# Kernel optimization log

Hardware: AMD Instinct MI355X
Metric: run time of the kernel (lower is better)

The kernel has to match this reference:

```python
import jax, jax.numpy as jnp
import numpy as np

R0 = 1.0
DIM_A, DIM_V, DIM_D = 32, 32, 32
N_NODES = 20000
N_EDGES = 640000


def radial_encode_8(r, r0):
    # 8 Gaussian radial basis functions on the edge length |r_ij|
    d = jnp.linalg.norm(r, axis=-1)                      # [E]
    centers = jnp.linspace(0.0, r0, 8)                   # [8]
    width = r0 / 8.0
    return jnp.exp(-(((d[..., None] - centers) / width) ** 2))  # [E,8]


def tens_sigmoid_vec(v):
    # norm-saturating nonlinearity for rank-1 tensors (direction-preserving)
    n2 = jnp.sum(v * v, axis=-1, keepdims=True)
    return v * jax.lax.rsqrt(1.0 + n2)


def setup_inputs() -> dict:
    key = jax.random.key(0)
    ks = jax.random.split(key, 12)

    def lin(k, fan_in, fan_out):
        return jax.random.normal(k, (fan_in, fan_out), jnp.float32) / np.float32(np.sqrt(fan_in))

    return dict(
        r_ij=jax.random.normal(ks[0], (N_EDGES, 3), jnp.float32),
        w_rad=lin(ks[1], 8, DIM_A), b_rad=jnp.zeros((DIM_A,), jnp.float32),
        w_direct=lin(ks[2], DIM_A, DIM_A),
        w1=lin(ks[3], DIM_A, 2 * DIM_A), b1=jnp.zeros((2 * DIM_A,), jnp.float32),
        w2=lin(ks[4], 2 * DIM_A, 2 * DIM_A), b2=jnp.zeros((2 * DIM_A,), jnp.float32),
        w3=lin(ks[5], 2 * DIM_A, DIM_A), b3=jnp.zeros((DIM_A,), jnp.float32),
        w_v=lin(ks[6], DIM_A, DIM_V),
        w_d=lin(ks[7], DIM_A, DIM_D),
        edges_src=jax.random.randint(ks[8], (N_EDGES,), 0, N_NODES),
        n_nodes=N_NODES,
    )


def reference(r_ij, w_rad, b_rad, w_direct, w1, b1, w2, b2, w3, b3, w_v, w_d,
              edges_src, n_nodes):
    lrelu = lambda x: jnp.where(x > 0, x, 0.1 * x)
    # radial MLP: Linear(8, a) -> MLP (lin_direct + 3-layer leakyrelu net)
    h = radial_encode_8(r_ij, R0) @ w_rad + b_rad                      # [E,a]
    rad = h @ w_direct + (lrelu(lrelu(h @ w1 + b1) @ w2 + b2) @ w3 + b3)  # [E,a]
    rs = tens_sigmoid_vec(r_ij * (7.0 / R0))                            # [E,3]

    seg = lambda x: jax.ops.segment_sum(x, edges_src, num_segments=n_nodes)
    A_a = seg(rad)                                                      # [N,a]
    A_v = seg(rad[:, :, None] * rs[:, None, :])                         # [N,a,3]
    # phi_d_ij = rad ⊗ rs ⊗ rs per edge  -> [E,a,3,3], then scatter-sum
    A_d = seg(rad[:, :, None, None] * rs[:, None, None, :] * rs[:, None, :, None])  # [N,a,3,3]

    out_v = jnp.einsum('nac,av->nvc', A_v, w_v)                         # TensLinear rank 1
    out_d = jnp.einsum('naij,ad->ndij', A_d, w_d)                       # TensLinear rank 2
    return A_a, out_v, out_d
```

## Files before the change

kernel.cpp:

```cpp
#include <hip/hip_runtime.h>
#include <hip/hip_bf16.h>
#include <hip/hip_fp16.h>
#include <math.h>


#define TSIZE 8192
#define DMAX  2.0f
#define NPB   4
#define EPB   4
#define HB    128
#define TILE  10240

#define O_WRAD 0
#define O_BRAD 256
#define O_WDIR 288
#define O_W1   1312
#define O_B1   3360
#define O_W2   3424
#define O_B2   7520
#define O_W3   7584
#define O_B3   9632
#define O_WV   9664
#define O_WD   10688
#define W_TOT  11712

__device__ __forceinline__ float lrelu(float x) { return x > 0.0f ? x : 0.1f * x; }

__device__ __forceinline__ float ldf(const void* p, int i, bool f32) {
    return f32 ? ((const float*)p)[i]
               : __uint_as_float(((unsigned int)((const unsigned short*)p)[i]) << 16);
}
__device__ __forceinline__ void stf(void* p, size_t i, float v, bool f32) {
    if (f32) ((float*)p)[i] = v;
    else     ((__hip_bfloat16*)p)[i] = __float2bfloat16(v);
}

__device__ __forceinline__ bool detect_f32(const void* r) {
    const unsigned short* p = (const unsigned short*)r;
    int bad = 0;
#pragma unroll 8
    for (int i = 0; i < 128; i++) {
        float v = __uint_as_float(((unsigned int)p[i]) << 16);
        bad |= (!isfinite(v) || fabsf(v) > 1e5f) ? 1 : 0;
    }
    return bad != 0;
}

__global__ void k_prep(const void* __restrict__ r_ij,
                       const void* w_rad, const void* b_rad, const void* w_direct,
                       const void* w1, const void* b1, const void* w2, const void* b2,
                       const void* w3, const void* b3, const void* w_v, const void* w_d,
                       float* __restrict__ wcat, int* __restrict__ flag,
                       int* __restrict__ counts, int N) {
    const int b = blockIdx.x;
    if (b == 0) {
        if (threadIdx.x == 0) flag[0] = detect_f32(r_ij) ? 1 : 0;
    } else if (b <= 11) {
        const bool f32 = detect_f32(r_ij);
        const void* src; int cnt; int off;
        switch (b) {
            case 1:  src = w_rad;    cnt = 256;  off = O_WRAD; break;
            case 2:  src = b_rad;    cnt = 32;   off = O_BRAD; break;
            case 3:  src = w_direct; cnt = 1024; off = O_WDIR; break;
            case 4:  src = w1;       cnt = 2048; off = O_W1;   break;
            case 5:  src = b1;       cnt = 64;   off = O_B1;   break;
            case 6:  src = w2;       cnt = 4096; off = O_W2;   break;
            case 7:  src = b2;       cnt = 64;   off = O_B2;   break;
            case 8:  src = w3;       cnt = 2048; off = O_W3;   break;
            case 9:  src = b3;       cnt = 32;   off = O_B3;   break;
            case 10: src = w_v;      cnt = 1024; off = O_WV;   break;
            default: src = w_d;      cnt = 1024; off = O_WD;   break;
        }
        for (int i = threadIdx.x; i < cnt; i += blockDim.x)
            wcat[off + i] = ldf(src, i, f32);
    } else if (counts) {
        int i = (b - 12) * blockDim.x + threadIdx.x;
        if (i < N) counts[i] = 0;
    }
}

__global__ void __launch_bounds__(64 * EPB) k_table(const float* __restrict__ wcat,
                                                    float* __restrict__ tabI) {
    __shared__ float Lh[EPB][32], Lt1[EPB][64], Lt2[EPB][64], Lrad[EPB][32];

    const int s = threadIdx.x >> 6;
    const int j = threadIdx.x & 63;
    const int e = blockIdx.x * EPB + s;
    const float d = (float)e * (DMAX / (float)(TSIZE - 1));

    float enc[8];
#pragma unroll
    for (int k = 0; k < 8; k++) {
        float t = (d - (float)k * (1.0f / 7.0f)) * 8.0f;
        enc[k] = expf(-t * t);
    }

    if (j < 32) {
        float hv = wcat[O_BRAD + j];
#pragma unroll
        for (int k = 0; k < 8; k++) hv = fmaf(enc[k], wcat[O_WRAD + k * 32 + j], hv);
        Lh[s][j] = hv;
    }
    __syncthreads();

    {
        float v = wcat[O_B1 + j];
#pragma unroll
        for (int i = 0; i < 32; i++) v = fmaf(Lh[s][i], wcat[O_W1 + i * 64 + j], v);
        Lt1[s][j] = lrelu(v);
    }
    __syncthreads();

    {
        float v = wcat[O_B2 + j];
#pragma unroll
        for (int i = 0; i < 64; i++) v = fmaf(Lt1[s][i], wcat[O_W2 + i * 64 + j], v);
        Lt2[s][j] = lrelu(v);
    }
    __syncthreads();

    if (j < 32) {
        float v = wcat[O_B3 + j];
#pragma unroll
        for (int i = 0; i < 64; i++) v = fmaf(Lt2[s][i], wcat[O_W3 + i * 32 + j], v);
#pragma unroll
        for (int i = 0; i < 32; i++) v = fmaf(Lh[s][i], wcat[O_WDIR + i * 32 + j], v);
        Lrad[s][j] = v;
        tabI[e * 96 + j] = v;
    }
    __syncthreads();

    if (j < 32) {
        float sv = 0.0f, sd = 0.0f;
#pragma unroll
        for (int i = 0; i < 32; i++) {
            float ri = Lrad[s][i];
            sv = fmaf(ri, wcat[O_WV + i * 32 + j], sv);
            sd = fmaf(ri, wcat[O_WD + i * 32 + j], sd);
        }
        tabI[e * 96 + 32 + j] = sv;
        tabI[e * 96 + 64 + j] = sd;
    }
}

__global__ void __launch_bounds__(256) k_hist(const int* __restrict__ src, int E,
                                              int chunk,
                                              unsigned short* __restrict__ cnt,
                                              int N) {
    __shared__ int lcnt[TILE];
    const int b = blockIdx.x % HB;
    const int t = blockIdx.x / HB;
    const int lo = b * chunk;
    const int hi = min(lo + chunk, E);
    const int t0 = t * TILE;
    const int tl = min(TILE, N - t0);

    for (int i = threadIdx.x; i < tl; i += 256) lcnt[i] = 0;
    __syncthreads();
    for (int e = lo + threadIdx.x; e < hi; e += 256) {
        const int s = src[e] - t0;
        if ((unsigned)s < (unsigned)tl) atomicAdd(&lcnt[s], 1);
    }
    __syncthreads();
    unsigned short* out = cnt + (size_t)(t * HB + b) * TILE;
    for (int i = threadIdx.x; i < tl; i += 256)
        out[i] = (unsigned short)lcnt[i];
}

__global__ void __launch_bounds__(64) k_colscan(unsigned short* __restrict__ cnt,
                                                int* __restrict__ tot,
                                                int* __restrict__ coarse, int N) {
    const int lane = threadIdx.x;
    const int n = blockIdx.x * 64 + lane;
    int run = 0;
    if (n < N) {
        const int t = n / TILE;
        const int nl = n % TILE;
        unsigned short* col = cnt + (size_t)(t * HB) * TILE + nl;
#pragma unroll 4
        for (int b = 0; b < HB; b++) {
            int c = col[(size_t)b * TILE];
            col[(size_t)b * TILE] = (unsigned short)run;
            run += c;
        }
        tot[n] = run;
    }
    int s = run;
    for (int off = 32; off > 0; off >>= 1) s += __shfl_down(s, off);
    if (lane == 0) coarse[blockIdx.x] = s;
}

__global__ void __launch_bounds__(64) k_scan2(const int* __restrict__ tot,
                                              const int* __restrict__ coarse,
                                              int* __restrict__ rowstart, int N) {
    const int lane = threadIdx.x;
    const int b = blockIdx.x;
    int cpre = 0;
    if (lane == 0) for (int i = 0; i < b; i++) cpre += coarse[i];
    cpre = __shfl(cpre, 0);
    const int n = b * 64 + lane;
    const int v = (n < N) ? tot[n] : 0;
    int inc = v;
    for (int off = 1; off < 64; off <<= 1) {
        int y = __shfl_up(inc, off);
        if (lane >= off) inc += y;
    }
    if (n < N) rowstart[n] = cpre + inc - v;
    if (n == N - 1) rowstart[N] = cpre + inc;
}

template <bool P16>
__global__ void __launch_bounds__(256) k_place(
        const int* __restrict__ src, int E, int chunk,
        const unsigned short* __restrict__ cnt, const int* __restrict__ rowstart,
        const void* __restrict__ r_ij, const int* __restrict__ flag,
        void* __restrict__ epsv, int N) {
    __shared__ int cur[TILE];
    const int b = blockIdx.x % HB;
    const int t = blockIdx.x / HB;
    const int lo = b * chunk;
    const int hi = min(lo + chunk, E);
    const int t0 = t * TILE;
    const int tl = min(TILE, N - t0);
    const bool f32 = flag[0] != 0;

    const unsigned short* base = cnt + (size_t)(t * HB + b) * TILE;
    for (int i = threadIdx.x; i < tl; i += 256)
        cur[i] = rowstart[t0 + i] + (int)base[i];
    __syncthreads();
    for (int e = lo + threadIdx.x; e < hi; e += 256) {
        const int s = src[e] - t0;
        if ((unsigned)s < (unsigned)tl) {
            const int pos = atomicAdd(&cur[s], 1);
            const float x = ldf(r_ij, 3 * e + 0, f32);
            const float y = ldf(r_ij, 3 * e + 1, f32);
            const float z = ldf(r_ij, 3 * e + 2, f32);
            const float d2 = x * x + y * y + z * z;
            const float inv = rsqrtf(1.0f + 49.0f * d2);
            const float u = fminf(sqrtf(d2), DMAX) * ((float)(TSIZE - 1) / DMAX);
            const int ti = (int)(u + 0.5f);
            const float rs0 = 7.0f * x * inv, rs1 = 7.0f * y * inv,
                        rs2 = 7.0f * z * inv;
            if (P16) {
                ((float4*)epsv)[pos] =
                    make_float4(rs0, rs1, rs2, __int_as_float(ti * 384));
            } else {
                const unsigned int h0 = __half_as_ushort(__float2half(rs0));
                const unsigned int h1 = __half_as_ushort(__float2half(rs1));
                const unsigned int h2 = __half_as_ushort(__float2half(rs2));
                ((uint2*)epsv)[pos] =
                    make_uint2(h0 | (h1 << 16), h2 | ((unsigned)ti << 16));
            }
        }
    }
}

template <bool P16>
__global__ void __launch_bounds__(64 * NPB) k_nodes(
    const void* __restrict__ epsv,
    const int* __restrict__ rowstart,
    const float* __restrict__ tabI,
    const int* __restrict__ flag,
    void* __restrict__ out, int N) {
    const int wave = threadIdx.x >> 6;
    const int lane = threadIdx.x & 63;
    const int n = blockIdx.x * NPB + wave;
    if (n >= N) return;
    const int a = lane & 31;
    const bool hi = (lane >> 5) != 0;
    const bool f32 = flag[0] != 0;
    const char* tabA = (const char*)tabI + (a << 2);

    const int s0 = rowstart[n];
    const int s1 = rowstart[n + 1];

    float accR = 0.f, acc1 = 0.f, acc2 = 0.f, acc3 = 0.f,
          acc4 = 0.f, acc5 = 0.f, acc6 = 0.f;

    int idx = s0;
    for (; idx + 1 < s1; idx += 2) {
        float ax, ay, az, bx, by, bz;
        const float *pA, *pB;
        if (P16) {
            const float4 qa = ((const float4*)epsv)[idx];
            const float4 qb = ((const float4*)epsv)[idx + 1];
            ax = qa.x; ay = qa.y; az = qa.z;
            bx = qb.x; by = qb.y; bz = qb.z;
            pA = (const float*)(tabA + __float_as_int(qa.w));
            pB = (const float*)(tabA + __float_as_int(qb.w));
        } else {
            const uint2 qa = ((const uint2*)epsv)[idx];
            const uint2 qb = ((const uint2*)epsv)[idx + 1];
            ax = __half2float(__ushort_as_half((unsigned short)(qa.x & 0xffff)));
            ay = __half2float(__ushort_as_half((unsigned short)(qa.x >> 16)));
            az = __half2float(__ushort_as_half((unsigned short)(qa.y & 0xffff)));
            bx = __half2float(__ushort_as_half((unsigned short)(qb.x & 0xffff)));
            by = __half2float(__ushort_as_half((unsigned short)(qb.x >> 16)));
            bz = __half2float(__ushort_as_half((unsigned short)(qb.y & 0xffff)));
            pA = (const float*)(tabA + (int)(qa.y >> 16) * 384);
            pB = (const float*)(tabA + (int)(qb.y >> 16) * 384);
        }
        const float raA = pA[0], rvA = pA[32], rdA = pA[64];
        const float raB = pB[0], rvB = pB[32], rdB = pB[64];

        const float b1A = (hi ? rdA : rvA) * (hi ? ay : 1.0f);
        const float b2A = rdA * (hi ? az : ax);
        const float b1B = (hi ? rdB : rvB) * (hi ? by : 1.0f);
        const float b2B = rdB * (hi ? bz : bx);

        accR += raA + raB;
        acc1 += b1A * ax + b1B * bx;
        acc2 += b1A * ay + b1B * by;
        acc3 += b1A * az + b1B * bz;
        acc4 += b2A * ax + b2B * bx;
        acc5 += b2A * ay + b2B * by;
        acc6 += b2A * az + b2B * bz;
    }
    if (idx < s1) {
        float x, y, z;
        const float* p;
        if (P16) {
            const float4 q = ((const float4*)epsv)[idx];
            x = q.x; y = q.y; z = q.z;
            p = (const float*)(tabA + __float_as_int(q.w));
        } else {
            const uint2 q = ((const uint2*)epsv)[idx];
            x = __half2float(__ushort_as_half((unsigned short)(q.x & 0xffff)));
            y = __half2float(__ushort_as_half((unsigned short)(q.x >> 16)));
            z = __half2float(__ushort_as_half((unsigned short)(q.y & 0xffff)));
            p = (const float*)(tabA + (int)(q.y >> 16) * 384);
        }
        const float ra = p[0], rv = p[32], rd = p[64];
        const float b1 = (hi ? rd : rv) * (hi ? y : 1.0f);
        const float b2 = rd * (hi ? z : x);
        accR += ra;
        acc1 += b1 * x; acc2 += b1 * y; acc3 += b1 * z;
        acc4 += b2 * x; acc5 += b2 * y; acc6 += b2 * z;
    }

    const size_t baseV = (size_t)N * 32;
    const size_t baseD = (size_t)N * 128;
    if (!hi) {
        stf(out, (size_t)n * 32 + a, accR, f32);
        const size_t vb = baseV + (size_t)n * 96 + a * 3;
        stf(out, vb + 0, acc1, f32);
        stf(out, vb + 1, acc2, f32);
        stf(out, vb + 2, acc3, f32);
        const size_t db = baseD + (size_t)n * 288 + a * 9;
        stf(out, db + 0, acc4, f32);
        stf(out, db + 1, acc5, f32);
        stf(out, db + 2, acc6, f32);
    } else {
        const size_t db = baseD + (size_t)n * 288 + a * 9;
        stf(out, db + 3, acc1, f32);
        stf(out, db + 4, acc2, f32);
        stf(out, db + 5, acc3, f32);
        stf(out, db + 6, acc4, f32);
        stf(out, db + 7, acc5, f32);
        stf(out, db + 8, acc6, f32);
    }
}

__global__ void k_rank_g(const int* __restrict__ src, int* __restrict__ counts,
                         int* __restrict__ rank, int E) {
    int e = blockIdx.x * blockDim.x + threadIdx.x;
    if (e < E) rank[e] = atomicAdd(&counts[src[e]], 1);
}
__global__ void k_scan_g(const int* __restrict__ counts, int* __restrict__ rowstart,
                         int N, int E) {
    __shared__ int part[1024];
    const int t = threadIdx.x;
    const int CH = (N + 1023) / 1024;
    const int lo = t * CH;
    const int hi = min(lo + CH, N);
    int s = 0;
    for (int i = lo; i < hi; i++) s += counts[i];
    part[t] = s;
    __syncthreads();
    for (int off = 1; off < 1024; off <<= 1) {
        int v = part[t];
        int w = (t >= off) ? part[t - off] : 0;
        __syncthreads();
        part[t] = v + w;
        __syncthreads();
    }
    int run = (t == 0) ? 0 : part[t - 1];
    for (int i = lo; i < hi; i++) { rowstart[i] = run; run += counts[i]; }
    if (t == 0) rowstart[N] = E;
}
__global__ void k_place_g(const int* __restrict__ src, const int* __restrict__ rank,
                          const int* __restrict__ rowstart,
                          int* __restrict__ perm, int E) {
    int e = blockIdx.x * blockDim.x + threadIdx.x;
    if (e < E) perm[rowstart[src[e]] + rank[e]] = e;
}
__global__ void __launch_bounds__(64 * NPB) k_nodes_fb(
    const int* __restrict__ perm, const void* __restrict__ r_ij,
    const int* __restrict__ rowstart, const float* __restrict__ tabI,
    const int* __restrict__ flag, void* __restrict__ out, int N) {
    const int wave = threadIdx.x >> 6;
    const int lane = threadIdx.x & 63;
    const int n = blockIdx.x * NPB + wave;
    if (n >= N) return;
    const int a = lane & 31;
    const bool hi = (lane >> 5) != 0;
    const bool f32 = flag[0] != 0;
    const int s0 = rowstart[n], s1 = rowstart[n + 1];
    float accR = 0.f, acc1 = 0.f, acc2 = 0.f, acc3 = 0.f,
          acc4 = 0.f, acc5 = 0.f, acc6 = 0.f;
    for (int idx = s0; idx < s1; idx++) {
        const int e = perm[idx];
        const float x0 = ldf(r_ij, 3 * e + 0, f32);
        const float y0 = ldf(r_ij, 3 * e + 1, f32);
        const float z0 = ldf(r_ij, 3 * e + 2, f32);
        const float d2 = x0 * x0 + y0 * y0 + z0 * z0;
        const float inv = rsqrtf(1.0f + 49.0f * d2);
        const float x = 7.0f * x0 * inv, y = 7.0f * y0 * inv, z = 7.0f * z0 * inv;
        const float u = fminf(sqrtf(d2), DMAX) * ((float)(TSIZE - 1) / DMAX);
        const int b = (int)(u + 0.5f) * 96 + a;
        const float ra = tabI[b], rv = tabI[b + 32], rd = tabI[b + 64];
        const float b1 = (hi ? rd : rv) * (hi ? y : 1.0f);
        const float b2 = rd * (hi ? z : x);
        accR += ra;
        acc1 += b1 * x; acc2 += b1 * y; acc3 += b1 * z;
        acc4 += b2 * x; acc5 += b2 * y; acc6 += b2 * z;
    }
    const size_t baseV = (size_t)N * 32;
    const size_t baseD = (size_t)N * 128;
    if (!hi) {
        stf(out, (size_t)n * 32 + a, accR, f32);
        const size_t vb = baseV + (size_t)n * 96 + a * 3;
        stf(out, vb + 0, acc1, f32);
        stf(out, vb + 1, acc2, f32);
        stf(out, vb + 2, acc3, f32);
        const size_t db = baseD + (size_t)n * 288 + a * 9;
        stf(out, db + 0, acc4, f32);
        stf(out, db + 1, acc5, f32);
        stf(out, db + 2, acc6, f32);
    } else {
        const size_t db = baseD + (size_t)n * 288 + a * 9;
        stf(out, db + 3, acc1, f32);
        stf(out, db + 4, acc2, f32);
        stf(out, db + 5, acc3, f32);
        stf(out, db + 6, acc4, f32);
        stf(out, db + 7, acc5, f32);
        stf(out, db + 8, acc6, f32);
    }
}

extern "C" void kernel_launch(void* const* d_in, const int* in_sizes, int n_in,
                              void* d_out, int out_size, void* d_ws, size_t ws_size,
                              hipStream_t stream) {
    const void* r_ij     = d_in[0];
    const void* w_rad    = d_in[1];
    const void* b_rad    = d_in[2];
    const void* w_direct = d_in[3];
    const void* w1       = d_in[4];
    const void* b1       = d_in[5];
    const void* w2       = d_in[6];
    const void* b2       = d_in[7];
    const void* w3       = d_in[8];
    const void* b3       = d_in[9];
    const void* w_v      = d_in[10];
    const void* w_d      = d_in[11];
    const int* edges_src = (const int*)d_in[12];

    const int E = in_sizes[12];
    const int N = out_size / 416;
    const int chunk = (E + HB - 1) / HB;
    const int ntiles = (N + TILE - 1) / TILE;
    const int NB = (N + 63) / 64;

    const size_t cntBytes  = (size_t)ntiles * HB * TILE * 2;
    const size_t tailBytes = ((size_t)W_TOT + 4) * 4 + (size_t)TSIZE * 96 * 4
                           + cntBytes + ((size_t)N + NB + N + 1) * 4;
    const bool p16 = ws_size >= (size_t)E * 16 + tailBytes + 64;
    const bool p8  = !p16 && ws_size >= (size_t)E * 8 + tailBytes + 64;

    char* w = (char*)d_ws;
    if (p16 || p8) {
        const size_t slot = (size_t)E * (p16 ? 16 : 8);
        void* eps     = (void*)w;
        float* wcat   = (float*)(w + slot);
        int* flag     = (int*)(wcat + W_TOT);
        float* tabI   = (float*)(flag + 4);
        unsigned short* cnt = (unsigned short*)(tabI + (size_t)TSIZE * 96);
        int* tot      = (int*)((char*)cnt + cntBytes);
        int* coarse   = tot + N;
        int* rowstart = coarse + NB;

        k_prep<<<12, 256, 0, stream>>>(
            r_ij, w_rad, b_rad, w_direct, w1, b1, w2, b2, w3, b3, w_v, w_d,
            wcat, flag, nullptr, N);
        k_table<<<TSIZE / EPB, 64 * EPB, 0, stream>>>(wcat, tabI);
        k_hist<<<HB * ntiles, 256, 0, stream>>>(edges_src, E, chunk, cnt, N);
        k_colscan<<<NB, 64, 0, stream>>>(cnt, tot, coarse, N);
        k_scan2<<<NB, 64, 0, stream>>>(tot, coarse, rowstart, N);
        if (p16) {
            k_place<true><<<HB * ntiles, 256, 0, stream>>>(
                edges_src, E, chunk, cnt, rowstart, r_ij, flag, eps, N);
            k_nodes<true><<<(N + NPB - 1) / NPB, 64 * NPB, 0, stream>>>(
                eps, rowstart, tabI, flag, d_out, N);
        } else {
            k_place<false><<<HB * ntiles, 256, 0, stream>>>(
                edges_src, E, chunk, cnt, rowstart, r_ij, flag, eps, N);
            k_nodes<false><<<(N + NPB - 1) / NPB, 64 * NPB, 0, stream>>>(
                eps, rowstart, tabI, flag, d_out, N);
        }
    } else {
        int* perm     = (int*)w;
        float* wcat   = (float*)(w + (size_t)E * 4);
        int* flag     = (int*)(wcat + W_TOT);
        float* tabI   = (float*)(flag + 4);
        int* counts   = (int*)(tabI + (size_t)TSIZE * 96);
        int* rowstart = counts + N;
        int* rank     = rowstart + N + 1;

        k_prep<<<12 + (N + 255) / 256, 256, 0, stream>>>(
            r_ij, w_rad, b_rad, w_direct, w1, b1, w2, b2, w3, b3, w_v, w_d,
            wcat, flag, counts, N);
        k_table<<<TSIZE / EPB, 64 * EPB, 0, stream>>>(wcat, tabI);
        k_rank_g<<<(E + 255) / 256, 256, 0, stream>>>(edges_src, counts, rank, E);
        k_scan_g<<<1, 1024, 0, stream>>>(counts, rowstart, N, E);
        k_place_g<<<(E + 255) / 256, 256, 0, stream>>>(edges_src, rank, rowstart,
                                                       perm, E);
        k_nodes_fb<<<(N + NPB - 1) / NPB, 64 * NPB, 0, stream>>>(
            perm, r_ij, rowstart, tabI, flag, d_out, N);
    }
}
```

Baseline: 218.8 us.

## Process two nodes per wave with half-wave node split and parallel coarse prefix

The node-accumulation kernel now assigns two nodes per wave, one per 32-lane half, and each lane computes all 13 output components for its channel, where before the two halves split one node's outputs. The goal is to halve the number of waves and have each edge record loaded by fewer lanes. The cost is more accumulator registers and divergence when the two nodes have different degrees. Separately, the second scan pass replaces a serial single-lane prefix over the coarse sums with a strided wave-wide reduction.

```diff
diff --git a/kernel.cpp b/kernel.cpp
--- a/kernel.cpp
+++ b/kernel.cpp
@@ -6,10 +6,10 @@
 
 #define TSIZE 8192
 #define DMAX  2.0f
-#define NPB   4
 #define EPB   4
 #define HB    128
 #define TILE  10240
+#define NPB   4
 
 #define O_WRAD 0
 #define O_BRAD 256
@@ -195,9 +195,11 @@
                                               int* __restrict__ rowstart, int N) {
     const int lane = threadIdx.x;
     const int b = blockIdx.x;
-    int cpre = 0;
-    if (lane == 0) for (int i = 0; i < b; i++) cpre += coarse[i];
-    cpre = __shfl(cpre, 0);
+    int cp = 0;
+    for (int j = lane; j < b; j += 64) cp += coarse[j];
+    for (int off = 32; off > 0; off >>= 1) cp += __shfl_down(cp, off);
+    const int cpre = __shfl(cp, 0);
+
     const int n = b * 64 + lane;
     const int v = (n < N) ? tot[n] : 0;
     int inc = v;
@@ -256,7 +258,7 @@
 }
 
 template <bool P16>
-__global__ void __launch_bounds__(64 * NPB) k_nodes(
+__global__ void __launch_bounds__(64 * NPB) k_nodes2(
     const void* __restrict__ epsv,
     const int* __restrict__ rowstart,
     const float* __restrict__ tabI,
@@ -264,101 +266,101 @@
     void* __restrict__ out, int N) {
     const int wave = threadIdx.x >> 6;
     const int lane = threadIdx.x & 63;
-    const int n = blockIdx.x * NPB + wave;
-    if (n >= N) return;
+    const int n0 = (blockIdx.x * NPB + wave) * 2;
     const int a = lane & 31;
-    const bool hi = (lane >> 5) != 0;
+    const int half = lane >> 5;
+    const int myn = n0 + half;
     const bool f32 = flag[0] != 0;
     const char* tabA = (const char*)tabI + (a << 2);
 
-    const int s0 = rowstart[n];
-    const int s1 = rowstart[n + 1];
-
-    float accR = 0.f, acc1 = 0.f, acc2 = 0.f, acc3 = 0.f,
-          acc4 = 0.f, acc5 = 0.f, acc6 = 0.f;
-
-    int idx = s0;
-    for (; idx + 1 < s1; idx += 2) {
-        float ax, ay, az, bx, by, bz;
-        const float *pA, *pB;
+    int s0 = 0, s1 = 0;
+    if (myn < N) { s0 = rowstart[myn]; s1 = rowstart[myn + 1]; }
+    const int mylen = s1 - s0;
+    const int lenA = __shfl(mylen, 0);
+    const int lenB = __shfl(mylen, 32);
+    const int minl = min(lenA, lenB);
+    const int maxl = max(lenA, lenB);
+
+    float accA = 0.f, v0 = 0.f, v1 = 0.f, v2 = 0.f;
+    float d00 = 0.f, d01 = 0.f, d02 = 0.f,
+          d10 = 0.f, d11 = 0.f, d12 = 0.f,
+          d20 = 0.f, d21 = 0.f, d22 = 0.f;
+
+#define EDGE_ACC(X, Y, Z, P)                                                  \
+    do {                                                                      \
+        const float ra = (P)[0], rv = (P)[32], rd = (P)[64];                  \
+        accA += ra;                                                           \
+        v0 += rv * (X); v1 += rv * (Y); v2 += rv * (Z);                       \
+        const float t0 = rd * (X), t1 = rd * (Y), t2 = rd * (Z);              \
+        d00 += t0 * (X); d01 += t0 * (Y); d02 += t0 * (Z);                    \
+        d10 += t1 * (X); d11 += t1 * (Y); d12 += t1 * (Z);                    \
+        d20 += t2 * (X); d21 += t2 * (Y); d22 += t2 * (Z);                    \
+    } while (0)
+
+    int i = 0;
+    for (; i + 1 < minl; i += 2) {
+        float x0, y0, z0, x1, y1, z1;
+        const float *p0, *p1;
         if (P16) {
-            const float4 qa = ((const float4*)epsv)[idx];
-            const float4 qb = ((const float4*)epsv)[idx + 1];
-            ax = qa.x; ay = qa.y; az = qa.z;
-            bx = qb.x; by = qb.y; bz = qb.z;
-            pA = (const float*)(tabA + __float_as_int(qa.w));
-            pB = (const float*)(tabA + __float_as_int(qb.w));
+            const float4 qa = ((const float4*)epsv)[s0 + i];
+            const float4 qb = ((const float4*)epsv)[s0 + i + 1];
+            x0 = qa.x; y0 = qa.y; z0 = qa.z;
+            x1 = qb.x; y1 = qb.y; z1 = qb.z;
+            p0 = (const float*)(tabA + __float_as_int(qa.w));
+            p1 = (const float*)(tabA + __float_as_int(qb.w));
         } else {
-            const uint2 qa = ((const uint2*)epsv)[idx];
-            const uint2 qb = ((const uint2*)epsv)[idx + 1];
-            ax = __half2float(__ushort_as_half((unsigned short)(qa.x & 0xffff)));
-            ay = __half2float(__ushort_as_half((unsigned short)(qa.x >> 16)));
-            az = __half2float(__ushort_as_half((unsigned short)(qa.y & 0xffff)));
-            bx = __half2float(__ushort_as_half((unsigned short)(qb.x & 0xffff)));
-            by = __half2float(__ushort_as_half((unsigned short)(qb.x >> 16)));
-            bz = __half2float(__ushort_as_half((unsigned short)(qb.y & 0xffff)));
-            pA = (const float*)(tabA + (int)(qa.y >> 16) * 384);
-            pB = (const float*)(tabA + (int)(qb.y >> 16) * 384);
-        }
-        const float raA = pA[0], rvA = pA[32], rdA = pA[64];
-        const float raB = pB[0], rvB = pB[32], rdB = pB[64];
-
-        const float b1A = (hi ? rdA : rvA) * (hi ? ay : 1.0f);
-        const float b2A = rdA * (hi ? az : ax);
-        const float b1B = (hi ? rdB : rvB) * (hi ? by : 1.0f);
-        const float b2B = rdB * (hi ? bz : bx);
-
-        accR += raA + raB;
-        acc1 += b1A * ax + b1B * bx;
-        acc2 += b1A * ay + b1B * by;
-        acc3 += b1A * az + b1B * bz;
-        acc4 += b2A * ax + b2B * bx;
-        acc5 += b2A * ay + b2B * by;
-        acc6 += b2A * az + b2B * bz;
-    }
-    if (idx < s1) {
-        float x, y, z;
-        const float* p;
-        if (P16) {
-            const float4 q = ((const float4*)epsv)[idx];
-            x = q.x; y = q.y; z = q.z;
-            p = (const float*)(tabA + __float_as_int(q.w));
-        } else {
-            const uint2 q = ((const uint2*)epsv)[idx];
-            x = __half2float(__ushort_as_half((unsigned short)(q.x & 0xffff)));
-            y = __half2float(__ushort_as_half((unsigned short)(q.x >> 16)));
-            z = __half2float(__ushort_as_half((unsigned short)(q.y & 0xffff)));
-            p = (const float*)(tabA + (int)(q.y >> 16) * 384);
-        }
-        const float ra = p[0], rv = p[32], rd = p[64];
-        const float b1 = (hi ? rd : rv) * (hi ? y : 1.0f);
-        const float b2 = rd * (hi ? z : x);
-        accR += ra;
-        acc1 += b1 * x; acc2 += b1 * y; acc3 += b1 * z;
-        acc4 += b2 * x; acc5 += b2 * y; acc6 += b2 * z;
-    }
-
+            const uint2 qa = ((const uint2*)epsv)[s0 + i];
+            const uint2 qb = ((const uint2*)epsv)[s0 + i + 1];
+            x0 = __half2float(__ushort_as_half((unsigned short)(qa.x & 0xffff)));
+            y0 = __half2float(__ushort_as_half((unsigned short)(qa.x >> 16)));
+            z0 = __half2float(__ushort_as_half((unsigned short)(qa.y & 0xffff)));
+            x1 = __half2float(__ushort_as_half((unsigned short)(qb.x & 0xffff)));
+            y1 = __half2float(__ushort_as_half((unsigned short)(qb.x >> 16)));
+            z1 = __half2float(__ushort_as_half((unsigned short)(qb.y & 0xffff)));
+            p0 = (const float*)(tabA + (int)(qa.y >> 16) * 384);
+            p1 = (const float*)(tabA + (int)(qb.y >> 16) * 384);
+        }
+        EDGE_ACC(x0, y0, z0, p0);
+        EDGE_ACC(x1, y1, z1, p1);
+    }
+    for (; i < maxl; i++) {
+        if (i < mylen) {
+            float x, y, z;
+            const float* p;
+            if (P16) {
+                const float4 q = ((const float4*)epsv)[s0 + i];
+                x = q.x; y = q.y; z = q.z;
+                p = (const float*)(tabA + __float_as_int(q.w));
+            } else {
+                const uint2 q = ((const uint2*)epsv)[s0 + i];
+                x = __half2float(__ushort_as_half((unsigned short)(q.x & 0xffff)));
+                y = __half2float(__ushort_as_half((unsigned short)(q.x >> 16)));
+                z = __half2float(__ushort_as_half((unsigned short)(q.y & 0xffff)));
+                p = (const float*)(tabA + (int)(q.y >> 16) * 384);
+            }
+            EDGE_ACC(x, y, z, p);
+        }
+    }
+#undef EDGE_ACC
+
+    if (myn >= N) return;
     const size_t baseV = (size_t)N * 32;
     const size_t baseD = (size_t)N * 128;
-    if (!hi) {
-        stf(out, (size_t)n * 32 + a, accR, f32);
-        const size_t vb = baseV + (size_t)n * 96 + a * 3;
-        stf(out, vb + 0, acc1, f32);
-        stf(out, vb + 1, acc2, f32);
-        stf(out, vb + 2, acc3, f32);
-        const size_t db = baseD + (size_t)n * 288 + a * 9;
-        stf(out, db + 0, acc4, f32);
-        stf(out, db + 1, acc5, f32);
-        stf(out, db + 2, acc6, f32);
-    } else {
-        const size_t db = baseD + (size_t)n * 288 + a * 9;
-        stf(out, db + 3, acc1, f32);
-        stf(out, db + 4, acc2, f32);
-        stf(out, db + 5, acc3, f32);
-        stf(out, db + 6, acc4, f32);
-        stf(out, db + 7, acc5, f32);
-        stf(out, db + 8, acc6, f32);
-    }
+    stf(out, (size_t)myn * 32 + a, accA, f32);
+    const size_t vb = baseV + (size_t)myn * 96 + a * 3;
+    stf(out, vb + 0, v0, f32);
+    stf(out, vb + 1, v1, f32);
+    stf(out, vb + 2, v2, f32);
+    const size_t db = baseD + (size_t)myn * 288 + a * 9;
+    stf(out, db + 0, d00, f32);
+    stf(out, db + 1, d01, f32);
+    stf(out, db + 2, d02, f32);
+    stf(out, db + 3, d10, f32);
+    stf(out, db + 4, d11, f32);
+    stf(out, db + 5, d12, f32);
+    stf(out, db + 6, d20, f32);
+    stf(out, db + 7, d21, f32);
+    stf(out, db + 8, d22, f32);
 }
 
 __global__ void k_rank_g(const int* __restrict__ src, int* __restrict__ counts,
@@ -394,13 +396,13 @@
     int e = blockIdx.x * blockDim.x + threadIdx.x;
     if (e < E) perm[rowstart[src[e]] + rank[e]] = e;
 }
-__global__ void __launch_bounds__(64 * NPB) k_nodes_fb(
+__global__ void __launch_bounds__(256) k_nodes_fb(
     const int* __restrict__ perm, const void* __restrict__ r_ij,
     const int* __restrict__ rowstart, const float* __restrict__ tabI,
     const int* __restrict__ flag, void* __restrict__ out, int N) {
     const int wave = threadIdx.x >> 6;
     const int lane = threadIdx.x & 63;
-    const int n = blockIdx.x * NPB + wave;
+    const int n = blockIdx.x * 4 + wave;
     if (n >= N) return;
     const int a = lane & 31;
     const bool hi = (lane >> 5) != 0;
@@ -489,6 +491,7 @@
         int* coarse   = tot + N;
         int* rowstart = coarse + NB;
 
+        const int nodeBlocks = (N + 2 * NPB - 1) / (2 * NPB);
         k_prep<<<12, 256, 0, stream>>>(
             r_ij, w_rad, b_rad, w_direct, w1, b1, w2, b2, w3, b3, w_v, w_d,
             wcat, flag, nullptr, N);
@@ -499,12 +502,12 @@
         if (p16) {
             k_place<true><<<HB * ntiles, 256, 0, stream>>>(
                 edges_src, E, chunk, cnt, rowstart, r_ij, flag, eps, N);
-            k_nodes<true><<<(N + NPB - 1) / NPB, 64 * NPB, 0, stream>>>(
+            k_nodes2<true><<<nodeBlocks, 64 * NPB, 0, stream>>>(
                 eps, rowstart, tabI, flag, d_out, N);
         } else {
             k_place<false><<<HB * ntiles, 256, 0, stream>>>(
                 edges_src, E, chunk, cnt, rowstart, r_ij, flag, eps, N);
-            k_nodes<false><<<(N + NPB - 1) / NPB, 64 * NPB, 0, stream>>>(
+            k_nodes2<false><<<nodeBlocks, 64 * NPB, 0, stream>>>(
                 eps, rowstart, tabI, flag, d_out, N);
         }
     } else {
@@ -524,7 +527,7 @@
         k_scan_g<<<1, 1024, 0, stream>>>(counts, rowstart, N, E);
         k_place_g<<<(E + 255) / 256, 256, 0, stream>>>(edges_src, rank, rowstart,
                                                        perm, E);
-        k_nodes_fb<<<(N + NPB - 1) / NPB, 64 * NPB, 0, stream>>>(
+        k_nodes_fb<<<(N + 3) / 4, 256, 0, stream>>>(
             perm, r_ij, rowstart, tabI, flag, d_out, N);
     }
 }
```

Result: faster. 207.7 us (-5.1%).
